# Kernel tuning notes

Measured on AMD Instinct MI355X. Metric: run time of the kernel, lower is better.

Reference implementation:

```python
import jax, jax.numpy as jnp
import numpy as np

N, T, D, H = 64, 512, 512, 512


def setup_inputs() -> dict:
    key = jax.random.key(0)
    k1, k2, k3, k4 = jax.random.split(key, 4)
    x = jax.random.normal(k1, (N, T, D), dtype=jnp.float32)
    h0 = jax.random.normal(k2, (N, H), dtype=jnp.float32)
    Wx = jax.random.normal(k3, (D, 4 * H), dtype=jnp.float32) / np.sqrt(D)
    Wh = jax.random.normal(k4, (H, 4 * H), dtype=jnp.float32) / np.sqrt(H)
    b = jnp.zeros((4 * H,), dtype=jnp.float32)
    return {"x": x, "h0": h0, "Wx": Wx, "Wh": Wh, "b": b}


def lstm_forward(x, h0, Wx, Wh, b):
    Hdim = h0.shape[1]
    # Precompute input-to-hidden projection for all timesteps: (N, T, 4H)
    xWx = jnp.einsum("ntd,dk->ntk", x, Wx) + b
    c0 = jnp.zeros_like(h0)

    def step(carry, a_x):
        prev_h, prev_c = carry
        a = a_x + prev_h @ Wh  # (N, 4H)
        i = jax.nn.sigmoid(a[:, :Hdim])
        f = jax.nn.sigmoid(a[:, Hdim:2 * Hdim])
        o = jax.nn.sigmoid(a[:, 2 * Hdim:3 * Hdim])
        g = jnp.tanh(a[:, 3 * Hdim:])
        next_c = f * prev_c + i * g
        next_h = o * jnp.tanh(next_c)
        return (next_h, next_c), next_h

    # scan over time: move T to leading axis
    _, hs = jax.lax.scan(step, (h0, c0), jnp.swapaxes(xWx, 0, 1))
    return jnp.swapaxes(hs, 0, 1)  # (N, T, H)


def reference(x, h0, Wx, Wh, b):
    return lstm_forward(x, h0, Wx, Wh, b)
```

## Files before the change

### kernel.cpp

```cpp
#include <hip/hip_runtime.h>
#include <hip/hip_bf16.h>

#define N_  64
#define T_  512
#define D_  512
#define H_  512
#define FH  2048
#define K1  1024
#define NWG 256
#define NSTEP 128
#define NHELP 128
#define BLK 256

typedef __attribute__((ext_vector_type(4))) float f32x4;
typedef __attribute__((ext_vector_type(8))) short bf16x8;

__device__ __forceinline__ unsigned short f2bf(float f) {
  unsigned u = __float_as_uint(f);
  return (unsigned short)((u + 0x7FFFu + ((u >> 16) & 1u)) >> 16);
}
__device__ __forceinline__ float bf2f(unsigned short s) {
  return __uint_as_float(((unsigned)s) << 16);
}
__device__ __forceinline__ float sigf(float x) {
  return 1.0f / (1.0f + __expf(-x));
}
__device__ __forceinline__ float tanhft(float x) {
  x = fminf(15.f, fmaxf(-15.f, x));
  float e = __expf(2.f * x);
  return (e - 1.f) / (e + 1.f);
}

__device__ __forceinline__ void gl_lds16(const void* g, void* l) {
  __builtin_amdgcn_global_load_lds(
      (const __attribute__((address_space(1))) void*)g,
      (__attribute__((address_space(3))) void*)l, 16, 0, 0);
}

__device__ __forceinline__ bf16x8 ld16cc(const short* p) {
  bf16x8 d;
  asm volatile("global_load_dwordx4 %0, %1, off sc0 sc1" : "=v"(d) : "v"(p));
  return d;
}
__device__ __forceinline__ void st4cc(short* p, unsigned v) {
  asm volatile("global_store_dword %0, %1, off sc0 sc1" ::"v"(p), "v"(v)
               : "memory");
}
__device__ __forceinline__ unsigned ldflag(const unsigned* p) {
  unsigned v;
  asm volatile("global_load_dword %0, %1, off sc0 sc1\ns_waitcnt vmcnt(0)"
               : "=v"(v) : "v"(p) : "memory");
  return v;
}
__device__ __forceinline__ void stflag(unsigned* p, unsigned v) {
  asm volatile("global_store_dword %0, %1, off sc0 sc1" ::"v"(p), "v"(v)
               : "memory");
}
__device__ __forceinline__ float ldf_cc(const float* p) {
  return __hip_atomic_load(p, __ATOMIC_RELAXED, __HIP_MEMORY_SCOPE_AGENT);
}

template <int SLP>
__device__ __forceinline__ void gbar2(unsigned* arr, unsigned* rel,
                                      unsigned gen, int wg) {
  __syncthreads();
  const int tid = threadIdx.x;
  if (tid == 0) {
    __builtin_amdgcn_fence(__ATOMIC_RELEASE, "agent");
    __hip_atomic_store(&arr[wg], gen, __ATOMIC_RELAXED,
                       __HIP_MEMORY_SCOPE_AGENT);
  }
  if (wg == 0) {
    if (tid < 64) {
      int guard = 0;
      for (;;) {
        unsigned v0 = __hip_atomic_load(&arr[tid], __ATOMIC_RELAXED,
                                        __HIP_MEMORY_SCOPE_AGENT);
        unsigned v1 = __hip_atomic_load(&arr[tid + 64], __ATOMIC_RELAXED,
                                        __HIP_MEMORY_SCOPE_AGENT);
        unsigned v2 = __hip_atomic_load(&arr[tid + 128], __ATOMIC_RELAXED,
                                        __HIP_MEMORY_SCOPE_AGENT);
        unsigned v3 = __hip_atomic_load(&arr[tid + 192], __ATOMIC_RELAXED,
                                        __HIP_MEMORY_SCOPE_AGENT);
        if (__all(v0 >= gen && v1 >= gen && v2 >= gen && v3 >= gen)) break;
        __builtin_amdgcn_s_sleep(SLP);
        if (++guard > (1 << 20)) break;
      }
    }
    __syncthreads();
    if (tid == 0)
      __hip_atomic_store(rel, gen, __ATOMIC_RELAXED, __HIP_MEMORY_SCOPE_AGENT);
  } else if (tid == 0) {
    int guard = 0;
    while (__hip_atomic_load(rel, __ATOMIC_RELAXED,
                             __HIP_MEMORY_SCOPE_AGENT) < gen) {
      __builtin_amdgcn_s_sleep(SLP);
      if (++guard > (1 << 20)) break;
    }
  }
  if (tid == 0) __builtin_amdgcn_fence(__ATOMIC_ACQUIRE, "agent");
  __syncthreads();
}

template <int SLP>
__device__ __forceinline__ void hbar(unsigned* arr, unsigned* rel,
                                     unsigned gen, int hid) {
  __syncthreads();
  const int tid = threadIdx.x;
  if (tid == 0) {
    __builtin_amdgcn_fence(__ATOMIC_RELEASE, "agent");
    __hip_atomic_store(&arr[hid], gen, __ATOMIC_RELAXED,
                       __HIP_MEMORY_SCOPE_AGENT);
  }
  if (hid == 0) {
    if (tid < 64) {
      int guard = 0;
      for (;;) {
        unsigned v0 = __hip_atomic_load(&arr[tid], __ATOMIC_RELAXED,
                                        __HIP_MEMORY_SCOPE_AGENT);
        unsigned v1 = __hip_atomic_load(&arr[tid + 64], __ATOMIC_RELAXED,
                                        __HIP_MEMORY_SCOPE_AGENT);
        if (__all(v0 >= gen && v1 >= gen)) break;
        __builtin_amdgcn_s_sleep(SLP);
        if (++guard > (1 << 20)) break;
      }
    }
    __syncthreads();
    if (tid == 0)
      __hip_atomic_store(rel, gen, __ATOMIC_RELAXED, __HIP_MEMORY_SCOPE_AGENT);
  } else if (tid == 0) {
    int guard = 0;
    while (__hip_atomic_load(rel, __ATOMIC_RELAXED,
                             __HIP_MEMORY_SCOPE_AGENT) < gen) {
      __builtin_amdgcn_s_sleep(SLP);
      if (++guard > (1 << 20)) break;
    }
  }
  if (tid == 0) __builtin_amdgcn_fence(__ATOMIC_ACQUIRE, "agent");
  __syncthreads();
}

__device__ __forceinline__ void convert_x(const float* __restrict__ x,
                                          short* __restrict__ xprim, int t0,
                                          int Mch, int idx0, int stride) {
  for (int idx = idx0; idx < Mch * 64; idx += stride) {
    int mrow = idx >> 6, oct = idx & 63;
    int tl = mrow >> 6, n = mrow & 63;
    const float* src = x + ((size_t)n * T_ + (t0 + tl)) * D_ + oct * 8;
    bf16x8 hv, lv;
#pragma unroll
    for (int i = 0; i < 8; ++i) {
      float v = src[i];
      unsigned short h = f2bf(v);
      hv[i] = (short)h;
      lv[i] = (short)f2bf(v - bf2f(h));
    }
    *(bf16x8*)(xprim + (size_t)mrow * K1 + oct * 8) = hv;
    *(bf16x8*)(xprim + (size_t)mrow * K1 + 512 + oct * 8) = lv;
  }
}

__device__ __forceinline__ void phase1(const short* __restrict__ xprim,
                                       const short* __restrict__ Wxt,
                                       const float* __restrict__ b,
                                       float* __restrict__ xw, int nTiles,
                                       int tile0, int tstride, short* Asm,
                                       short* Bsm) {
  const int tid = threadIdx.x;
  const int lane = tid & 63, wv = tid >> 6;
  const int wm = wv >> 1, wn = wv & 1;
  const int sslot = (lane & 3) ^ ((lane >> 3) & 3);
  for (int tile = tile0; tile < nTiles; tile += tstride) {
    int tm = tile >> 4, tn = tile & 15;
    int m0 = tm << 7, n0 = tn << 7;
    f32x4 acc[4][4];
    for (int i = 0; i < 4; ++i)
      for (int j = 0; j < 4; ++j) acc[i][j] = (f32x4){0.f, 0.f, 0.f, 0.f};
    for (int kk = 0; kk < 48; ++kk) {
      int ac = (kk < 16 ? kk : kk - 16) << 5;
      int bc = (kk < 32 ? kk : kk - 32) << 5;
      __syncthreads();
      {
        const short* sa =
            xprim + (size_t)(m0 + wv * 32 + (lane >> 2)) * K1 + ac + sslot * 8;
        gl_lds16(sa, Asm + (wv * 32) * 32);
        gl_lds16(sa + (size_t)16 * K1, Asm + (wv * 32 + 16) * 32);
        const short* sb =
            Wxt + (size_t)(n0 + wv * 32 + (lane >> 2)) * K1 + bc + sslot * 8;
        gl_lds16(sb, Bsm + (wv * 32) * 32);
        gl_lds16(sb + (size_t)16 * K1, Bsm + (wv * 32 + 16) * 32);
      }
      __syncthreads();
      bf16x8 af[4], bfr[4];
      for (int mi = 0; mi < 4; ++mi) {
        int R = wm * 64 + mi * 16 + (lane & 15);
        int rs = ((lane >> 4) & 3) ^ ((R >> 1) & 3);
        af[mi] = *(const bf16x8*)(Asm + R * 32 + rs * 8);
      }
      for (int ni = 0; ni < 4; ++ni) {
        int R = wn * 64 + ni * 16 + (lane & 15);
        int rs = ((lane >> 4) & 3) ^ ((R >> 1) & 3);
        bfr[ni] = *(const bf16x8*)(Bsm + R * 32 + rs * 8);
      }
      for (int mi = 0; mi < 4; ++mi)
        for (int ni = 0; ni < 4; ++ni)
          acc[mi][ni] = __builtin_amdgcn_mfma_f32_16x16x32_bf16(
              af[mi], bfr[ni], acc[mi][ni], 0, 0, 0);
    }
    for (int ni = 0; ni < 4; ++ni) {
      float bj = b[n0 + wn * 64 + ni * 16 + (lane & 15)];
      for (int mi = 0; mi < 4; ++mi) {
        int mg = m0 + wm * 64 + mi * 16 + ((lane >> 4) << 2);
        float* dst = xw + (size_t)mg * FH + n0 + wn * 64 + ni * 16 + (lane & 15);
        for (int r = 0; r < 4; ++r) dst[(size_t)r * FH] = acc[mi][ni][r] + bj;
      }
    }
  }
}

__device__ __forceinline__ void run_steps(
    int rb, int cg, int t0, int Tc, unsigned& fl, float& creg,
    const short* __restrict__ Wht, short* hbuf0, short* hbuf1,
    const float* __restrict__ xw, float* __restrict__ out, unsigned* arrH,
    unsigned* cdone, int chIdx, short* hst, float (*glds)[16][16]) {
  const int tid = threadIdx.x;
  const int lane = tid & 63, wv = tid >> 6;
  const int row = tid >> 4, col = tid & 15;
  const int n = rb * 16 + row, jh = cg * 16 + col;
  unsigned* myflag = &arrH[rb * 32 + cg];
  unsigned* grp = &arrH[rb * 32];
  short* hstLo = hst + 16 * 512;

  bf16x8 bW[32];
  {
    const int gcl = wv * 512 + cg * 16 + (lane & 15);
#pragma unroll
    for (int kk = 0; kk < 32; ++kk)
      bW[kk] = *(const bf16x8*)(Wht + (size_t)gcl * K1 + kk * 32 +
                                (lane >> 4) * 8);
  }

  const float* xr0 = xw + ((size_t)n) * FH + jh;
  float x0 = ldf_cc(xr0), x1 = ldf_cc(xr0 + 512), x2 = ldf_cc(xr0 + 1024),
        x3 = ldf_cc(xr0 + 1536);

  for (int tl = 0; tl < Tc; ++tl) {
    const int tg = t0 + tl;
    if (wv == 0) {
      int guard = 0;
      for (;;) {
        unsigned v = ldflag(grp + (lane & 31));
        if (__all(v >= fl)) break;
        __builtin_amdgcn_s_sleep(1);
        if (++guard > (1 << 20)) break;
      }
    }
    __syncthreads();
    if (tl == 0 && cg == 0 && tid == 0) stflag(cdone, (unsigned)chIdx);

    const short* hc = (tg & 1) ? hbuf1 : hbuf0;
    short* hn = (tg & 1) ? hbuf0 : hbuf1;

    bf16x8 tmp[8];
#pragma unroll
    for (int i = 0; i < 4; ++i) {
      int r = i * 4 + wv;
      tmp[i] = ld16cc(hc + (size_t)(rb * 16 + r) * K1 + lane * 8);
    }
#pragma unroll
    for (int i = 0; i < 4; ++i) {
      int r = i * 4 + wv;
      tmp[4 + i] = ld16cc(hc + (size_t)(rb * 16 + r) * K1 + 512 + lane * 8);
    }
    asm volatile("s_waitcnt vmcnt(0)" ::: "memory");
    __builtin_amdgcn_sched_barrier(0);
#pragma unroll
    for (int i = 0; i < 4; ++i) {
      int r = i * 4 + wv;
      *(bf16x8*)(hst + r * 512 + ((lane ^ (r & 7)) << 3)) = tmp[i];
      *(bf16x8*)(hstLo + r * 512 + ((lane ^ (r & 7)) << 3)) = tmp[4 + i];
    }
    __syncthreads();

    bf16x8 af[16];
#pragma unroll
    for (int kk = 0; kk < 16; ++kk) {
      int c = kk * 4 + (lane >> 4), r = lane & 15;
      af[kk] = *(const bf16x8*)(hst + r * 512 + ((c ^ (r & 7)) << 3));
    }
    f32x4 acc0 = {0.f, 0.f, 0.f, 0.f};
    f32x4 acc1 = {0.f, 0.f, 0.f, 0.f};
#pragma unroll
    for (int kk = 0; kk < 32; ++kk) {
      if (kk & 1)
        acc1 = __builtin_amdgcn_mfma_f32_16x16x32_bf16(af[kk & 15], bW[kk],
                                                       acc1, 0, 0, 0);
      else
        acc0 = __builtin_amdgcn_mfma_f32_16x16x32_bf16(af[kk & 15], bW[kk],
                                                       acc0, 0, 0, 0);
    }
#pragma unroll
    for (int kk = 0; kk < 16; ++kk) {
      int c = kk * 4 + (lane >> 4), r = lane & 15;
      bf16x8 al = *(const bf16x8*)(hstLo + r * 512 + ((c ^ (r & 7)) << 3));
      if (kk & 1)
        acc1 = __builtin_amdgcn_mfma_f32_16x16x32_bf16(al, bW[kk], acc1, 0, 0, 0);
      else
        acc0 = __builtin_amdgcn_mfma_f32_16x16x32_bf16(al, bW[kk], acc0, 0, 0, 0);
    }
    f32x4 a = acc0 + acc1;
    for (int r = 0; r < 4; ++r)
      glds[wv][((lane >> 4) << 2) + r][lane & 15] = a[r];
    __syncthreads();
    float hv;
    {
      float gi = glds[0][row][col] + x0;
      float gf = glds[1][row][col] + x1;
      float go = glds[2][row][col] + x2;
      float gg = glds[3][row][col] + x3;
      float si = sigf(gi), sf = sigf(gf), so = sigf(go);
      float tg2 = tanhft(gg);
      float cn = sf * creg + si * tg2;
      creg = cn;
      hv = so * tanhft(cn);
      unsigned short hi2 = f2bf(hv);
      unsigned short lo2 = f2bf(hv - bf2f(hi2));
      unsigned ohi = (unsigned)__shfl_xor((int)(unsigned)hi2, 1);
      unsigned olo = (unsigned)__shfl_xor((int)(unsigned)lo2, 1);
      if (col & 1)
        st4cc(hn + (size_t)n * K1 + 512 + (jh - 1),
              olo | ((unsigned)lo2 << 16));
      else
        st4cc(hn + (size_t)n * K1 + jh, (unsigned)hi2 | (ohi << 16));
    }
    asm volatile("s_waitcnt vmcnt(0)" ::: "memory");
    __syncthreads();
    if (tid == 0) stflag(myflag, fl + 1);
    out[((size_t)n * T_ + tg) * H_ + jh] = hv;
    if (tl + 1 < Tc) {
      const float* xr = xw + ((size_t)(tl + 1) * 64 + n) * FH + jh;
      x0 = ldf_cc(xr); x1 = ldf_cc(xr + 512);
      x2 = ldf_cc(xr + 1024); x3 = ldf_cc(xr + 1536);
    }
    ++fl;
  }
}

__global__ void __launch_bounds__(BLK, 1)
lstm_persistent(const float* __restrict__ x, const float* __restrict__ h0,
                const float* __restrict__ Wx, const float* __restrict__ Wh,
                const float* __restrict__ b, float* __restrict__ out,
                void* __restrict__ ws, int Tc) {
  __shared__ __align__(16) short sbuf[16384];
  __shared__ float glds[4][16][16];

  char* wsb = (char*)ws;
  unsigned* relF   = (unsigned*)(wsb + 0);
  unsigned* chrdy  = (unsigned*)(wsb + 64);
  unsigned* cdone  = (unsigned*)(wsb + 128);
  unsigned* arrF   = (unsigned*)(wsb + 256);
  unsigned* relJ   = (unsigned*)(wsb + 1280);
  unsigned* arrJ   = (unsigned*)(wsb + 1344);
  unsigned* arrH   = (unsigned*)(wsb + 2048);
  short* Wxt   = (short*)(wsb + 4096);
  short* Wht   = Wxt + (size_t)FH * K1;
  short* hbuf0 = Wht + (size_t)FH * K1;
  short* hbuf1 = hbuf0 + N_ * K1;
  float* cbuf  = (float*)(hbuf1 + N_ * K1);
  short* xprim = (short*)(cbuf + N_ * H_);
  float* xwxb  = (float*)(xprim + (size_t)Tc * N_ * K1);

  const int tid = threadIdx.x;
  const int wg = blockIdx.x;
  const int gtid = wg * BLK + tid;
  const bool isStep = (wg & 7) < 4;
  const int rb = wg & 7;
  const int cg = wg >> 3;
  const int hid = (wg >> 3) * 4 + ((wg & 7) - 4);

  unsigned genF = 0, genJ = 0, fl = 0;

  for (int idx = gtid; idx < 2 * FH * 64; idx += NWG * BLK) {
    int m = idx >> 17;
    int rr = idx & 131071;
    int j = rr >> 6;
    int oct = rr & 63;
    const float* W = m ? Wh : Wx;
    bf16x8 hv, lv;
#pragma unroll
    for (int i = 0; i < 8; ++i) {
      float v = W[(size_t)(oct * 8 + i) * FH + j];
      unsigned short h = f2bf(v);
      hv[i] = (short)h;
      lv[i] = (short)f2bf(v - bf2f(h));
    }
    short* dst = m ? Wht : Wxt;
    *(bf16x8*)(dst + (size_t)j * K1 + oct * 8) = hv;
    *(bf16x8*)(dst + (size_t)j * K1 + 512 + oct * 8) = lv;
  }
  for (int idx = gtid; idx < N_ * H_; idx += NWG * BLK) {
    int n = idx >> 9, k = idx & 511;
    float v = h0[idx];
    unsigned short hi = f2bf(v);
    unsigned short lo = f2bf(v - bf2f(hi));
    hbuf0[n * K1 + k] = (short)hi;
    hbuf0[n * K1 + 512 + k] = (short)lo;
  }
  gbar2<4>(arrF, relF, ++genF, wg);

  const int nCh = T_ / Tc;
  const int Mch = Tc * N_;
  const int nTiles = (Mch >> 7) * (FH >> 7);
  const size_t xwStride = (size_t)Mch * FH;

  convert_x(x, xprim, 0, Mch, gtid, NWG * BLK);
  gbar2<2>(arrF, relF, ++genF, wg);
  phase1(xprim, Wxt, b, xwxb, nTiles, wg, NWG, sbuf, sbuf + 4096);
  gbar2<2>(arrF, relF, ++genF, wg);

  if (isStep) {
    float creg = 0.0f;
    for (int ch = 0; ch < nCh; ++ch) {
      if (ch > 0) {
        if (tid == 0) {
          int guard = 0;
          while (ldflag(chrdy) < (unsigned)ch) {
            __builtin_amdgcn_s_sleep(8);
            if (++guard > (1 << 20)) break;
          }
        }
        __syncthreads();
      }
      run_steps(rb, cg, ch * Tc, Tc, fl, creg, Wht, hbuf0, hbuf1,
                xwxb + (size_t)(ch & 1) * xwStride, out, arrH, &cdone[rb], ch,
                sbuf, glds);
    }
  } else {
    for (int ch = 0; ch + 1 < nCh; ++ch) {
      if (ch > 0) {
        if (tid == 0) {
          int guard = 0;
          for (;;) {
            unsigned d0 = ldflag(&cdone[0]);
            unsigned d1 = ldflag(&cdone[1]);
            unsigned d2 = ldflag(&cdone[2]);
            unsigned d3 = ldflag(&cdone[3]);
            if (d0 >= (unsigned)ch && d1 >= (unsigned)ch &&
                d2 >= (unsigned)ch && d3 >= (unsigned)ch)
              break;
            __builtin_amdgcn_s_sleep(16);
            if (++guard > (1 << 20)) break;
          }
        }
        __syncthreads();
      }
      convert_x(x, xprim, (ch + 1) * Tc, Mch, hid * BLK + tid, NHELP * BLK);
      hbar<1>(arrJ, relJ, ++genJ, hid);
      phase1(xprim, Wxt, b, xwxb + (size_t)((ch + 1) & 1) * xwStride, nTiles,
             hid, NHELP, sbuf, sbuf + 4096);
      hbar<1>(arrJ, relJ, ++genJ, hid);
      if (hid == 0 && tid == 0) stflag(chrdy, (unsigned)(ch + 1));
    }
  }
}

extern "C" void kernel_launch(void* const* d_in, const int* in_sizes, int n_in,
                              void* d_out, int out_size, void* d_ws, size_t ws_size,
                              hipStream_t stream) {
  (void)in_sizes; (void)n_in; (void)out_size;
  const float* x  = (const float*)d_in[0];
  const float* h0 = (const float*)d_in[1];
  const float* Wx = (const float*)d_in[2];
  const float* Wh = (const float*)d_in[3];
  const float* b  = (const float*)d_in[4];
  float* out = (float*)d_out;

  size_t fixed = 4096 + 2 * (size_t)FH * K1 * 2 + 2 * (size_t)N_ * K1 * 2 +
                 (size_t)N_ * H_ * 4;
  size_t perTc = (size_t)N_ * K1 * 2 + 2 * (size_t)N_ * FH * 4;
  int Tc = 64;
  while (Tc > 1 && fixed + (size_t)Tc * perTc > ws_size) Tc >>= 1;

  (void)hipMemsetAsync(d_ws, 0, 4096, stream);

  void* args[] = {(void*)&x, (void*)&h0, (void*)&Wx, (void*)&Wh,
                  (void*)&b, (void*)&out, (void*)&d_ws, (void*)&Tc};

  hipError_t e = hipLaunchCooperativeKernel((void*)lstm_persistent, dim3(NWG),
                                            dim3(BLK), args, 0, stream);
  if (e != hipSuccess) {
    (void)hipGetLastError();
    lstm_persistent<<<dim3(NWG), dim3(BLK), 0, stream>>>(x, h0, Wx, Wh, b,
                                                         out, d_ws, Tc);
    (void)hipGetLastError();
  }
}
```

Before: 1.788 ms.

## Replace per-step flag barrier with canary-tagged 4-buffer hidden-state polling

Drops the per-timestep arrival-flag synchronization between step workgroups. Instead, h is kept in a 4-deep ring of buffers, and consumers poll the data itself until no canary sentinel values remain. After each step, producers write the new h and re-poison the buffer from two steps back with canaries. This removes a flag store, a syncthreads and a separate flag poll from each step, at the cost of repeated full-data reloads while spinning. It also depends on correct memory ordering between the data stores and the canary stores, and assumes no legitimate h value encodes as the canary pattern.

```diff
diff --git a/kernel.cpp b/kernel.cpp
--- a/kernel.cpp
+++ b/kernel.cpp
@@ -11,9 +11,11 @@
 #define NSTEP 128
 #define NHELP 128
 #define BLK 256
+#define CANARY 0xFFFFFFFFu
 
 typedef __attribute__((ext_vector_type(4))) float f32x4;
 typedef __attribute__((ext_vector_type(8))) short bf16x8;
+typedef __attribute__((ext_vector_type(4))) unsigned u32x4;
 
 __device__ __forceinline__ unsigned short f2bf(float f) {
   unsigned u = __float_as_uint(f);
@@ -219,17 +221,16 @@
 }
 
 __device__ __forceinline__ void run_steps(
-    int rb, int cg, int t0, int Tc, unsigned& fl, float& creg,
-    const short* __restrict__ Wht, short* hbuf0, short* hbuf1,
-    const float* __restrict__ xw, float* __restrict__ out, unsigned* arrH,
+    int rb, int cg, int t0, int Tc, float& creg,
+    const short* __restrict__ Wht, short* hb,
+    const float* __restrict__ xw, float* __restrict__ out,
     unsigned* cdone, int chIdx, short* hst, float (*glds)[16][16]) {
   const int tid = threadIdx.x;
   const int lane = tid & 63, wv = tid >> 6;
   const int row = tid >> 4, col = tid & 15;
   const int n = rb * 16 + row, jh = cg * 16 + col;
-  unsigned* myflag = &arrH[rb * 32 + cg];
-  unsigned* grp = &arrH[rb * 32];
   short* hstLo = hst + 16 * 512;
+  const size_t hbs = (size_t)N_ * K1;
 
   bf16x8 bW[32];
   {
@@ -246,34 +247,34 @@
 
   for (int tl = 0; tl < Tc; ++tl) {
     const int tg = t0 + tl;
-    if (wv == 0) {
+    const short* hc = hb + (size_t)(tg & 3) * hbs;
+    short* hn = hb + (size_t)((tg + 1) & 3) * hbs;
+    short* hp = hb + (size_t)((tg + 3) & 3) * hbs;
+
+    bf16x8 tmp[8];
+    {
       int guard = 0;
       for (;;) {
-        unsigned v = ldflag(grp + (lane & 31));
-        if (__all(v >= fl)) break;
-        __builtin_amdgcn_s_sleep(1);
+#pragma unroll
+        for (int i = 0; i < 4; ++i) {
+          int r = i * 4 + wv;
+          tmp[i] = ld16cc(hc + (size_t)(rb * 16 + r) * K1 + lane * 8);
+          tmp[4 + i] = ld16cc(hc + (size_t)(rb * 16 + r) * K1 + 512 + lane * 8);
+        }
+        asm volatile("s_waitcnt vmcnt(0)" ::: "memory");
+        __builtin_amdgcn_sched_barrier(0);
+        bool ok = true;
+#pragma unroll
+        for (int i = 0; i < 8; ++i) {
+          u32x4 u = *(const u32x4*)&tmp[i];
+          ok = ok && (u[0] != CANARY) && (u[1] != CANARY) &&
+               (u[2] != CANARY) && (u[3] != CANARY);
+        }
+        if (__all(ok)) break;
+        __builtin_amdgcn_s_sleep(0);
         if (++guard > (1 << 20)) break;
       }
     }
-    __syncthreads();
-    if (tl == 0 && cg == 0 && tid == 0) stflag(cdone, (unsigned)chIdx);
-
-    const short* hc = (tg & 1) ? hbuf1 : hbuf0;
-    short* hn = (tg & 1) ? hbuf0 : hbuf1;
-
-    bf16x8 tmp[8];
-#pragma unroll
-    for (int i = 0; i < 4; ++i) {
-      int r = i * 4 + wv;
-      tmp[i] = ld16cc(hc + (size_t)(rb * 16 + r) * K1 + lane * 8);
-    }
-#pragma unroll
-    for (int i = 0; i < 4; ++i) {
-      int r = i * 4 + wv;
-      tmp[4 + i] = ld16cc(hc + (size_t)(rb * 16 + r) * K1 + 512 + lane * 8);
-    }
-    asm volatile("s_waitcnt vmcnt(0)" ::: "memory");
-    __builtin_amdgcn_sched_barrier(0);
 #pragma unroll
     for (int i = 0; i < 4; ++i) {
       int r = i * 4 + wv;
@@ -281,6 +282,7 @@
       *(bf16x8*)(hstLo + r * 512 + ((lane ^ (r & 7)) << 3)) = tmp[4 + i];
     }
     __syncthreads();
+    if (tl == 0 && cg == 0 && tid == 0) stflag(cdone, (unsigned)chIdx);
 
     bf16x8 af[16];
 #pragma unroll
@@ -327,22 +329,23 @@
       unsigned short lo2 = f2bf(hv - bf2f(hi2));
       unsigned ohi = (unsigned)__shfl_xor((int)(unsigned)hi2, 1);
       unsigned olo = (unsigned)__shfl_xor((int)(unsigned)lo2, 1);
+      asm volatile("s_waitcnt vmcnt(0)" ::: "memory");
       if (col & 1)
         st4cc(hn + (size_t)n * K1 + 512 + (jh - 1),
               olo | ((unsigned)lo2 << 16));
       else
         st4cc(hn + (size_t)n * K1 + jh, (unsigned)hi2 | (ohi << 16));
-    }
-    asm volatile("s_waitcnt vmcnt(0)" ::: "memory");
-    __syncthreads();
-    if (tid == 0) stflag(myflag, fl + 1);
+      if (col & 1)
+        st4cc(hp + (size_t)n * K1 + 512 + (jh - 1), CANARY);
+      else
+        st4cc(hp + (size_t)n * K1 + jh, CANARY);
+    }
     out[((size_t)n * T_ + tg) * H_ + jh] = hv;
     if (tl + 1 < Tc) {
       const float* xr = xw + ((size_t)(tl + 1) * 64 + n) * FH + jh;
       x0 = ldf_cc(xr); x1 = ldf_cc(xr + 512);
       x2 = ldf_cc(xr + 1024); x3 = ldf_cc(xr + 1536);
     }
-    ++fl;
   }
 }
 
@@ -361,13 +364,10 @@
   unsigned* arrF   = (unsigned*)(wsb + 256);
   unsigned* relJ   = (unsigned*)(wsb + 1280);
   unsigned* arrJ   = (unsigned*)(wsb + 1344);
-  unsigned* arrH   = (unsigned*)(wsb + 2048);
   short* Wxt   = (short*)(wsb + 4096);
   short* Wht   = Wxt + (size_t)FH * K1;
-  short* hbuf0 = Wht + (size_t)FH * K1;
-  short* hbuf1 = hbuf0 + N_ * K1;
-  float* cbuf  = (float*)(hbuf1 + N_ * K1);
-  short* xprim = (short*)(cbuf + N_ * H_);
+  short* hb    = Wht + (size_t)FH * K1;
+  short* xprim = hb + 4 * (size_t)N_ * K1;
   float* xwxb  = (float*)(xprim + (size_t)Tc * N_ * K1);
 
   const int tid = threadIdx.x;
@@ -378,7 +378,7 @@
   const int cg = wg >> 3;
   const int hid = (wg >> 3) * 4 + ((wg & 7) - 4);
 
-  unsigned genF = 0, genJ = 0, fl = 0;
+  unsigned genF = 0, genJ = 0;
 
   for (int idx = gtid; idx < 2 * FH * 64; idx += NWG * BLK) {
     int m = idx >> 17;
@@ -403,8 +403,13 @@
     float v = h0[idx];
     unsigned short hi = f2bf(v);
     unsigned short lo = f2bf(v - bf2f(hi));
-    hbuf0[n * K1 + k] = (short)hi;
-    hbuf0[n * K1 + 512 + k] = (short)lo;
+    hb[n * K1 + k] = (short)hi;
+    hb[n * K1 + 512 + k] = (short)lo;
+  }
+  {
+    unsigned* pz = (unsigned*)(hb + (size_t)N_ * K1);
+    for (int idx = gtid; idx < 3 * N_ * K1 / 2; idx += NWG * BLK)
+      pz[idx] = CANARY;
   }
   gbar2<4>(arrF, relF, ++genF, wg);
 
@@ -431,8 +436,8 @@
         }
         __syncthreads();
       }
-      run_steps(rb, cg, ch * Tc, Tc, fl, creg, Wht, hbuf0, hbuf1,
-                xwxb + (size_t)(ch & 1) * xwStride, out, arrH, &cdone[rb], ch,
+      run_steps(rb, cg, ch * Tc, Tc, creg, Wht, hb,
+                xwxb + (size_t)(ch & 1) * xwStride, out, &cdone[rb], ch,
                 sbuf, glds);
     }
   } else {
@@ -475,8 +480,7 @@
   const float* b  = (const float*)d_in[4];
   float* out = (float*)d_out;
 
-  size_t fixed = 4096 + 2 * (size_t)FH * K1 * 2 + 2 * (size_t)N_ * K1 * 2 +
-                 (size_t)N_ * H_ * 4;
+  size_t fixed = 4096 + 2 * (size_t)FH * K1 * 2 + 4 * (size_t)N_ * K1 * 2;
   size_t perTc = (size_t)N_ * K1 * 2 + 2 * (size_t)N_ * FH * 4;
   int Tc = 64;
   while (Tc > 1 && fixed + (size_t)Tc * perTc > ws_size) Tc >>= 1;
```

After: 2.283 ms. +27.7%, slower.
